# Optimization experiments

Hardware: AMD Instinct MI355X
Metric: run time of the kernel (lower is better)

Reference implementation:

```python
import jax, jax.numpy as jnp
import numpy as np

D = 64       # d_model (channel)
NHEAD = 8    # heads in nn.MultiheadAttention
PROTO = 16   # proto_size == num_queries
EPS = 1e-5


def _haar_filters():
    L = np.array([1.0, 1.0], np.float32) / np.float32(np.sqrt(2.0))
    H = np.array([-1.0, 1.0], np.float32) / np.float32(np.sqrt(2.0))
    # WavePool: LL, LH, HL, HH Haar filters (2x2, stride 2, depthwise)
    return [jnp.asarray(np.outer(a, b)) for (a, b) in ((L, L), (L, H), (H, L), (H, H))]


def _dw(x, k2d, stride):
    # depthwise conv with the SAME 2D filter per channel; x: [B,C,H,W]
    C = x.shape[1]
    k = jnp.tile(k2d[None, None], (C, 1, 1, 1)).astype(x.dtype)
    return jax.lax.conv_general_dilated(x, k, (stride, stride), 'VALID',
        dimension_numbers=('NCHW', 'OIHW', 'NCHW'), feature_group_count=C)


def _ln(x, g, b):
    m = jnp.mean(x, -1, keepdims=True)
    v = jnp.var(x, -1, keepdims=True)
    return (x - m) * jax.lax.rsqrt(v + EPS) * g + b


def _bn(x, g, b, m, v):
    # eval-mode BatchNorm2d, x: [B,C,H,W]
    sh = (1, -1, 1, 1)
    return (x - m.reshape(sh)) * jax.lax.rsqrt(v.reshape(sh) + EPS) * g.reshape(sh) + b.reshape(sh)


def _mscw(x, lw1, lb1, lw2, lb2, gw1, gb1, gw2, gb2):
    pool = jnp.mean(x, axis=1, keepdims=True)            # [B,1,C]
    loc = jax.nn.relu(x @ lw1.T + lb1) @ lw2.T + lb2
    glo = jax.nn.relu(pool @ gw1.T + gb1) @ gw2.T + gb2
    return jax.nn.sigmoid(loc + glo)


def _mha(q, k, v, w_in, b_in, w_out, b_out):
    # standard nn.MultiheadAttention (batch_first), q:[B,Nq,D], k/v:[B,Nk,D]
    B, Nq, d = q.shape
    dk = d // NHEAD
    qp = q @ w_in[:d].T + b_in[:d]
    kp = k @ w_in[d:2 * d].T + b_in[d:2 * d]
    vp = v @ w_in[2 * d:].T + b_in[2 * d:]
    split = lambda t: t.reshape(t.shape[0], t.shape[1], NHEAD, dk).transpose(0, 2, 1, 3)
    qh, kh, vh = split(qp), split(kp), split(vp)
    scores = jnp.einsum('bhqd,bhkd->bhqk', qh, kh) * (1.0 / np.sqrt(dk))
    attn = jax.nn.softmax(scores, axis=-1)
    o = jnp.einsum('bhqk,bhkd->bhqd', attn, vh).transpose(0, 2, 1, 3).reshape(B, Nq, d)
    return o @ w_out.T + b_out


def reference(tgt, memory, pos, query_pos,
              w_in, b_in, w_out, b_out,
              ln1_g, ln1_b, ln2_g, ln2_b,
              m1_lw1, m1_lb1, m1_lw2, m1_lb2, m1_gw1, m1_gb1, m1_gw2, m1_gb2,
              m2_lw1, m2_lb1, m2_lw2, m2_lb2, m2_gw1, m2_gb1, m2_gw2, m2_gb2,
              dw_w, bn1_g, bn1_b, bn1_m, bn1_v, pw_w, bn2_g, bn2_b, bn2_m, bn2_v,
              mheads_w):
    # CrossAttentionLayer.forward_post -> custom MultiheadAttention.forward
    query = (tgt + query_pos).transpose(1, 0, 2)   # [B,Nq,C]
    key = (memory + pos).transpose(1, 0, 2)        # [B,N1,C]
    value = memory.transpose(1, 0, 2)
    B, N1, C = value.shape
    hw = int(np.sqrt(N1))
    feat = key.transpose(0, 2, 1).reshape(B, C, hw, hw)
    fLL, fLH, fHL, fHH = _haar_filters()
    LL = _dw(feat, fLL, 2)
    LH = _dw(feat, fLH, 2)
    HL = _dw(feat, fHL, 2)
    HH = _dw(feat, fHH, 2)
    high = (HL + LH + HH).reshape(B, C, -1).transpose(0, 2, 1)  # [B,N1/4,C]
    low = LL.reshape(B, C, -1).transpose(0, 2, 1)
    wei = _mscw(high + low, m1_lw1, m1_lb1, m1_lw2, m1_lb2, m1_gw1, m1_gb1, m1_gw2, m1_gb2)
    fre = wei * high + low
    x1 = _mha(query, fre, fre, w_in, b_in, w_out, b_out)
    x1 = _ln(x1 + query, ln1_g, ln1_b)
    # DSConv3x3: depthwise 3x3 + BN + ReLU, then 1x1 + BN + ReLU
    y = jax.lax.conv_general_dilated(feat, dw_w, (1, 1), ((1, 1), (1, 1)),
        dimension_numbers=('NCHW', 'OIHW', 'NCHW'), feature_group_count=C)
    y = jax.nn.relu(_bn(y, bn1_g, bn1_b, bn1_m, bn1_v))
    y = jax.lax.conv_general_dilated(y, pw_w, (1, 1), 'VALID',
        dimension_numbers=('NCHW', 'OIHW', 'NCHW'))
    y = jax.nn.relu(_bn(y, bn2_g, bn2_b, bn2_m, bn2_v))
    featf = y.reshape(B, C, -1).transpose(0, 2, 1)          # [B,N1,C]
    mw = jax.nn.softmax(featf @ mheads_w.T, axis=1)          # softmax over tokens, [B,N1,P]
    protos = jnp.einsum('bnp,bnc->bpc', mw, key)             # [B,P,C]
    attn2 = _mscw(protos + query, m2_lw1, m2_lb1, m2_lw2, m2_lb2, m2_gw1, m2_gb1, m2_gw2, m2_gb2)
    x2 = _ln(query * attn2 + query, ln2_g, ln2_b)
    return (x1 + x2).transpose(1, 0, 2)                      # [Nq,B,C]


def setup_inputs() -> dict:
    key = jax.random.key(0)
    ks = iter(jax.random.split(key, 40))
    B, HW, NQ = 8, 128, PROTO
    N1 = HW * HW
    wn = lambda *s: jax.random.normal(next(ks), s, jnp.float32) * 0.05
    inp = {
        'tgt': jax.random.normal(next(ks), (NQ, B, D), jnp.float32),
        'memory': jax.random.normal(next(ks), (N1, B, D), jnp.float32),
        'pos': jax.random.normal(next(ks), (N1, B, D), jnp.float32),
        'query_pos': jax.random.normal(next(ks), (NQ, B, D), jnp.float32),
        'w_in': wn(3 * D, D), 'b_in': jnp.zeros((3 * D,), jnp.float32),
        'w_out': wn(D, D), 'b_out': jnp.zeros((D,), jnp.float32),
        'ln1_g': jnp.ones((D,), jnp.float32), 'ln1_b': jnp.zeros((D,), jnp.float32),
        'ln2_g': jnp.ones((D,), jnp.float32), 'ln2_b': jnp.zeros((D,), jnp.float32),
        'dw_w': wn(D, 1, 3, 3),
        'bn1_g': jnp.ones((D,), jnp.float32), 'bn1_b': jnp.zeros((D,), jnp.float32),
        'bn1_m': jnp.zeros((D,), jnp.float32), 'bn1_v': jnp.ones((D,), jnp.float32),
        'pw_w': wn(D, D, 1, 1),
        'bn2_g': jnp.ones((D,), jnp.float32), 'bn2_b': jnp.zeros((D,), jnp.float32),
        'bn2_m': jnp.zeros((D,), jnp.float32), 'bn2_v': jnp.ones((D,), jnp.float32),
        'mheads_w': wn(PROTO, D),
    }
    for pfx in ('m1', 'm2'):
        for br in ('l', 'g'):
            inp[f'{pfx}_{br}w1'] = wn(D, D)
            inp[f'{pfx}_{br}b1'] = jnp.zeros((D,), jnp.float32)
            inp[f'{pfx}_{br}w2'] = wn(D, D)
            inp[f'{pfx}_{br}b2'] = jnp.zeros((D,), jnp.float32)
    return inp
```

## Files before the change

### kernel.cpp

```cpp
#include <hip/hip_runtime.h>
#include <math.h>

#define N1 16384
#define N2 4096

#define OFF_KEY   0L
#define OFF_KPH   4194304L
#define OFF_VPH   5242880L
#define OFF_WB    6291456L
#define OFF_CST   6302208L
#define OFF_POOL  6331648L
#define OFF_PROT  6332160L
#define OFF_ZZ    6340352L
#define OFF_QP    6340480L
#define OFF_QB    6348672L
#define OFF_PART  6356864L

typedef __attribute__((ext_vector_type(8))) short bf16x8;
typedef __attribute__((ext_vector_type(4))) float floatx4;

#define MFMA16(a, b, c) __builtin_amdgcn_mfma_f32_16x16x32_bf16(a, b, c, 0, 0, 0)

__device__ __forceinline__ unsigned short f2bf(float f) {
    union { float f; unsigned u; } v; v.f = f;
    unsigned r = v.u + 0x7fffu + ((v.u >> 16) & 1u);
    return (unsigned short)(r >> 16);
}
__device__ __forceinline__ float bf2f(unsigned short s) {
    union { unsigned u; float f; } v; v.u = ((unsigned)s) << 16;
    return v.f;
}
__device__ __forceinline__ float sigmoidf_(float x) { return 1.f / (1.f + __expf(-x)); }
__device__ __forceinline__ bf16x8 ldg8b(const unsigned short* p) { return *(const bf16x8*)p; }
__device__ __forceinline__ void unpack8(uint4 v, float* f) {
    f[0] = bf2f((unsigned short)(v.x & 0xffff)); f[1] = bf2f((unsigned short)(v.x >> 16));
    f[2] = bf2f((unsigned short)(v.y & 0xffff)); f[3] = bf2f((unsigned short)(v.y >> 16));
    f[4] = bf2f((unsigned short)(v.z & 0xffff)); f[5] = bf2f((unsigned short)(v.z >> 16));
    f[6] = bf2f((unsigned short)(v.w & 0xffff)); f[7] = bf2f((unsigned short)(v.w >> 16));
}

__global__ __launch_bounds__(256) void k_stage1(
        const float* __restrict__ mem, const float* __restrict__ pos,
        const float* __restrict__ m1lw1, const float* __restrict__ m1lw2,
        const float* __restrict__ w_in, const float* __restrict__ pw,
        const float* __restrict__ mh, const float* __restrict__ dw_w,
        const float* __restrict__ bn1_g, const float* __restrict__ bn1_b,
        const float* __restrict__ bn1_m, const float* __restrict__ bn1_v,
        const float* __restrict__ bn2_g, const float* __restrict__ bn2_b,
        const float* __restrict__ bn2_m, const float* __restrict__ bn2_v,
        const float* __restrict__ m1gw1, const float* __restrict__ m1gw2,
        const float* __restrict__ m2gw1, const float* __restrict__ m2gw2,
        const float* __restrict__ m2lw1, const float* __restrict__ m2lw2,
        const float* __restrict__ w_out,
        const float* __restrict__ tgt, const float* __restrict__ qpos,
        const float* __restrict__ b_in,
        unsigned short* __restrict__ key, float* __restrict__ pool1raw,
        unsigned short* __restrict__ wb, float* __restrict__ cst,
        float* __restrict__ qp, float* __restrict__ queryb) {
    int tid = threadIdx.x;
    if (blockIdx.x < 4096) {
        __shared__ float sh[16][64];
        int b = blockIdx.x >> 9;
        int n_base = (blockIdx.x & 511) * 32;
        int c8 = tid & 7, local_n = tid >> 3;
        int n = n_base + local_n;
        long s4 = ((long)n * 8 + b) * 16 + c8 * 2;
        float4 m0 = ((const float4*)mem)[s4], m1 = ((const float4*)mem)[s4 + 1];
        float4 p0 = ((const float4*)pos)[s4], p1 = ((const float4*)pos)[s4 + 1];
        float f[8];
        f[0] = m0.x + p0.x; f[1] = m0.y + p0.y; f[2] = m0.z + p0.z; f[3] = m0.w + p0.w;
        f[4] = m1.x + p1.x; f[5] = m1.y + p1.y; f[6] = m1.z + p1.z; f[7] = m1.w + p1.w;
        uint4 o;
        o.x = (unsigned)f2bf(f[0]) | ((unsigned)f2bf(f[1]) << 16);
        o.y = (unsigned)f2bf(f[2]) | ((unsigned)f2bf(f[3]) << 16);
        o.z = (unsigned)f2bf(f[4]) | ((unsigned)f2bf(f[5]) << 16);
        o.w = (unsigned)f2bf(f[6]) | ((unsigned)f2bf(f[7]) << 16);
        ((uint4*)key)[(long)(b * 16384 + n) * 8 + c8] = o;
        int parity = (n_base >> 7) & 1;
        if (parity) {
            if (local_n & 1) {
                #pragma unroll
                for (int j = 0; j < 8; j++) sh[local_n >> 1][c8 * 8 + j] = f[j];
            }
            __syncthreads();
            if (tid < 64) {
                float s = 0.f;
                #pragma unroll
                for (int k = 0; k < 16; k++) s += sh[k][tid];
                atomicAdd(pool1raw + b * 64 + tid, s);
            }
        }
        return;
    }
    int blk = blockIdx.x - 4096;
    if (blk < 84) {
        int i = blk * 256 + tid;
        float v;
        if (i < 4096) v = m1lw1[i];
        else if (i < 8192) v = m1lw2[i - 4096];
        else if (i < 16384) v = w_in[4096 + (i - 8192)];
        else if (i < 20480) v = pw[i - 16384];
        else v = mh[i - 20480];
        wb[i] = f2bf(v);
    } else if (blk < 199) {
        int j = (blk - 84) * 256 + tid;
        float v;
        if (j < 576) {
            int k = j >> 6, c = j & 63;
            float s1 = bn1_g[c] * rsqrtf(bn1_v[c] + 1e-5f);
            v = dw_w[c * 9 + k] * s1;
        } else if (j < 640) {
            int c = j - 576;
            float s1 = bn1_g[c] * rsqrtf(bn1_v[c] + 1e-5f);
            v = bn1_b[c] - bn1_m[c] * s1;
        } else if (j < 704) {
            int c = j - 640;
            v = bn2_g[c] * rsqrtf(bn2_v[c] + 1e-5f);
        } else if (j < 768) {
            int c = j - 704;
            float s2 = bn2_g[c] * rsqrtf(bn2_v[c] + 1e-5f);
            v = bn2_b[c] - bn2_m[c] * s2;
        } else {
            int jj = j - 768;
            int m = jj >> 12, idx = jj & 4095;
            int sidx = (idx & 63) * 64 + (idx >> 6);
            const float* src;
            switch (m) {
                case 0: src = m1gw1; break;
                case 1: src = m1gw2; break;
                case 2: src = m2gw1; break;
                case 3: src = m2gw2; break;
                case 4: src = m2lw1; break;
                case 5: src = m2lw2; break;
                default: src = w_out; break;
            }
            v = src[sidx];
        }
        cst[j] = v;
    } else {
        __shared__ float qv[4][64];
        int g = tid >> 6, lane = tid & 63;
        int u = (blk - 199) * 4 + g;
        int b = u >> 4, q = u & 15;
        long src = ((long)q * 8 + b) * 64 + lane;
        float v = tgt[src] + qpos[src];
        qv[g][lane] = v;
        queryb[(b * 16 + q) * 64 + lane] = v;
        __syncthreads();
        float acc = b_in[lane];
        for (int cc = 0; cc < 64; cc++) acc += qv[g][cc] * w_in[lane * 64 + cc];
        qp[(b * 16 + q) * 64 + lane] = acc;
    }
}

__global__ __launch_bounds__(512) void k_stage2(
        const unsigned short* __restrict__ keyb,
        const float* __restrict__ pool1raw,
        const float* __restrict__ lb1, const float* __restrict__ lb2,
        const float* __restrict__ gb1, const float* __restrict__ gb2,
        const float* __restrict__ b_in,
        const unsigned short* __restrict__ wb,
        const float* __restrict__ cst,
        unsigned short* __restrict__ kph, unsigned short* __restrict__ vph,
        float* __restrict__ protos, float* __restrict__ Z) {
    __shared__ __align__(16) char smem[63488];
    int tid = threadIdx.x;
    int w = tid >> 6, l = tid & 63;
    if (blockIdx.x < 512) {
        short* stage = (short*)smem;
        short* hbuf  = (short*)(smem + 36864);
        short* wbuf  = (short*)(smem + 46080);
        float* parr  = (float*)(smem + 55296);
        float* gtmp  = parr + 64;
        float* gbuf  = parr + 128;
        int b = blockIdx.x >> 6, tile = blockIdx.x & 63;
        int pairw = w >> 1, ch2 = w & 1;
        int m0 = pairw * 16, trow = l & 15, oct = l >> 4;
        const float* gw1T = cst + 768;
        const float* gw2T = cst + 4864;
        if (tid < 64) parr[tid] = pool1raw[b * 64 + tid] * (2.0f / 4096.0f);
        const unsigned short* src = keyb + ((long)b * 16384 + tile * 256) * 64;
        #pragma unroll
        for (int k = 0; k < 4; k++) {
            int u = k * 512 + tid;
            int p = u >> 3, o = u & 7;
            uint4 v = *(const uint4*)(src + (long)u * 8);
            *(uint4*)(stage + p * 72 + o * 8) = v;
        }
        __syncthreads();
        if (tid < 64) {
            float a = gb1[tid];
            for (int cc = 0; cc < 64; cc++) a += parr[cc] * gw1T[cc * 64 + tid];
            gtmp[tid] = fmaxf(a, 0.f);
        }
        int j = m0 + trow;
        float x[16], S[16];
        bf16x8 ax[2];
        #pragma unroll
        for (int half = 0; half < 2; half++) {
            int o = oct + half * 4;
            uint4 fa4 = *(const uint4*)(stage + (2 * j) * 72 + o * 8);
            uint4 fb4 = *(const uint4*)(stage + (2 * j + 1) * 72 + o * 8);
            uint4 fc4 = *(const uint4*)(stage + (128 + 2 * j) * 72 + o * 8);
            uint4 fd4 = *(const uint4*)(stage + (129 + 2 * j) * 72 + o * 8);
            float A[8], B[8], C[8], D[8];
            unpack8(fa4, A); unpack8(fb4, B); unpack8(fc4, C); unpack8(fd4, D);
            #pragma unroll
            for (int jj = 0; jj < 8; jj++) {
                float xd = 2.f * D[jj];
                x[half * 8 + jj] = xd;
                S[half * 8 + jj] = 0.5f * (A[jj] + B[jj] + C[jj] + D[jj]);
                ax[half][jj] = (short)f2bf(xd);
            }
        }
        const unsigned short* w1b = wb;
        const unsigned short* w2b = wb + 4096;
        const unsigned short* wkb = wb + 8192;
        const unsigned short* wvb = wb + 12288;
        #pragma unroll
        for (int t4i = 0; t4i < 2; t4i++) {
            int n = (ch2 * 2 + t4i) * 16 + trow;
            float bias = lb1[n];
            floatx4 acc = {bias, bias, bias, bias};
            acc = MFMA16(ax[0], ldg8b(w1b + n * 64 + oct * 8), acc);
            acc = MFMA16(ax[1], ldg8b(w1b + n * 64 + 32 + oct * 8), acc);
            #pragma unroll
            for (int r = 0; r < 4; r++)
                hbuf[(m0 + oct * 4 + r) * 72 + n] = (short)f2bf(fmaxf(acc[r], 0.f));
        }
        __syncthreads();
        if (tid < 64) {
            float g = gb2[tid];
            for (int hh = 0; hh < 64; hh++) g += gtmp[hh] * gw2T[hh * 64 + tid];
            gbuf[tid] = g;
        }
        __syncthreads();
        {
            bf16x8 ah0 = *(const bf16x8*)(hbuf + (m0 + trow) * 72 + oct * 8);
            bf16x8 ah1 = *(const bf16x8*)(hbuf + (m0 + trow) * 72 + 32 + oct * 8);
            #pragma unroll
            for (int t4i = 0; t4i < 2; t4i++) {
                int n = (ch2 * 2 + t4i) * 16 + trow;
                float bias = lb2[n];
                floatx4 acc = {bias, bias, bias, bias};
                acc = MFMA16(ah0, ldg8b(w2b + n * 64 + oct * 8), acc);
                acc = MFMA16(ah1, ldg8b(w2b + n * 64 + 32 + oct * 8), acc);
                float g = gbuf[n];
                #pragma unroll
                for (int r = 0; r < 4; r++)
                    wbuf[(m0 + oct * 4 + r) * 72 + n] = (short)f2bf(sigmoidf_(acc[r] + g));
            }
        }
        __syncthreads();
        bf16x8 af0, af1;
        {
            bf16x8 w0 = *(const bf16x8*)(wbuf + (m0 + trow) * 72 + oct * 8);
            bf16x8 w1v = *(const bf16x8*)(wbuf + (m0 + trow) * 72 + 32 + oct * 8);
            #pragma unroll
            for (int jj = 0; jj < 8; jj++) {
                float we0 = bf2f((unsigned short)w0[jj]);
                float we1 = bf2f((unsigned short)w1v[jj]);
                af0[jj] = (short)f2bf(we0 * x[jj] + (1.f - we0) * S[jj]);
                af1[jj] = (short)f2bf(we1 * x[8 + jj] + (1.f - we1) * S[8 + jj]);
            }
        }
        __syncthreads();
        short* kbuf = hbuf; short* vbuf = wbuf;
        #pragma unroll
        for (int t4i = 0; t4i < 2; t4i++) {
            int ko = (ch2 * 2 + t4i) * 16 + trow;
            float bk = b_in[64 + ko], bv = b_in[128 + ko];
            floatx4 ak = {bk, bk, bk, bk};
            floatx4 av = {bv, bv, bv, bv};
            ak = MFMA16(af0, ldg8b(wkb + ko * 64 + oct * 8), ak);
            ak = MFMA16(af1, ldg8b(wkb + ko * 64 + 32 + oct * 8), ak);
            av = MFMA16(af0, ldg8b(wvb + ko * 64 + oct * 8), av);
            av = MFMA16(af1, ldg8b(wvb + ko * 64 + 32 + oct * 8), av);
            #pragma unroll
            for (int r = 0; r < 4; r++) {
                int row = m0 + oct * 4 + r;
                kbuf[row * 72 + ko] = (short)f2bf(ak[r]);
                vbuf[row * 72 + ko] = (short)f2bf(av[r]);
            }
        }
        __syncthreads();
        {
            int h = tid >> 6, tok = tid & 63;
            uint4 kk = *(const uint4*)(kbuf + tok * 72 + h * 8);
            uint4 vv = *(const uint4*)(vbuf + tok * 72 + h * 8);
            long du = (long)(b * 8 + h) * 4096 + tile * 64 + tok;
            ((uint4*)kph)[du] = kk;
            ((uint4*)vph)[du] = vv;
        }
        return;
    }
    {
        short* stage = (short*)smem;
        short* pbuf  = (short*)(smem + 55296);
        float* cbuf  = (float*)(smem + 55296 + 4352);
        float* zred  = (float*)(smem + 55296 + 4352 + 3072);
        int blk = blockIdx.x - 512;
        int b = blk >> 7, h = blk & 127;
        int p0 = w * 16, pr = l & 15, oct = l >> 4;
        for (int k = tid; k < 768; k += 512) cbuf[k] = cst[k];
        const unsigned short* kb = keyb + (long)b * 1048576;
        #pragma unroll
        for (int r = 0; r < 3; r++) {
            int row = h - 1 + r;
            if ((unsigned)row < 128u) {
                const unsigned short* src = kb + (long)row * 8192;
                #pragma unroll
                for (int k = 0; k < 2; k++) {
                    int u = k * 512 + tid;
                    int p = u >> 3, o = u & 7;
                    uint4 v = *(const uint4*)(src + (long)u * 8);
                    *(uint4*)(stage + (r * 128 + p) * 72 + o * 8) = v;
                }
            } else {
                uint4 zz = {0u, 0u, 0u, 0u};
                #pragma unroll
                for (int k = 0; k < 2; k++) {
                    int u = k * 512 + tid;
                    int p = u >> 3, o = u & 7;
                    *(uint4*)(stage + (r * 128 + p) * 72 + o * 8) = zz;
                }
            }
        }
        __syncthreads();
        float accf[2][8];
        #pragma unroll
        for (int half = 0; half < 2; half++)
            #pragma unroll
            for (int jj = 0; jj < 8; jj++) accf[half][jj] = 0.f;
        #pragma unroll
        for (int r = 0; r < 3; r++) {
            #pragma unroll
            for (int kk = 0; kk < 3; kk++) {
                int col = p0 + pr - 1 + kk;
                if ((unsigned)col < 128u) {
                    #pragma unroll
                    for (int half = 0; half < 2; half++) {
                        int o = oct + half * 4;
                        uint4 d4 = *(const uint4*)(stage + (r * 128 + col) * 72 + o * 8);
                        float f[8]; unpack8(d4, f);
                        float4 wa = *(const float4*)(cbuf + (r * 3 + kk) * 64 + o * 8);
                        float4 wc = *(const float4*)(cbuf + (r * 3 + kk) * 64 + o * 8 + 4);
                        accf[half][0] += f[0] * wa.x; accf[half][1] += f[1] * wa.y;
                        accf[half][2] += f[2] * wa.z; accf[half][3] += f[3] * wa.w;
                        accf[half][4] += f[4] * wc.x; accf[half][5] += f[5] * wc.y;
                        accf[half][6] += f[6] * wc.z; accf[half][7] += f[7] * wc.w;
                    }
                }
            }
        }
        bf16x8 af[2];
        #pragma unroll
        for (int half = 0; half < 2; half++) {
            int o = oct + half * 4;
            float4 oa = *(const float4*)(cbuf + 576 + o * 8);
            float4 ob = *(const float4*)(cbuf + 576 + o * 8 + 4);
            af[half][0] = (short)f2bf(fmaxf(accf[half][0] + oa.x, 0.f));
            af[half][1] = (short)f2bf(fmaxf(accf[half][1] + oa.y, 0.f));
            af[half][2] = (short)f2bf(fmaxf(accf[half][2] + oa.z, 0.f));
            af[half][3] = (short)f2bf(fmaxf(accf[half][3] + oa.w, 0.f));
            af[half][4] = (short)f2bf(fmaxf(accf[half][4] + ob.x, 0.f));
            af[half][5] = (short)f2bf(fmaxf(accf[half][5] + ob.y, 0.f));
            af[half][6] = (short)f2bf(fmaxf(accf[half][6] + ob.z, 0.f));
            af[half][7] = (short)f2bf(fmaxf(accf[half][7] + ob.w, 0.f));
        }
        __syncthreads();
        short* y2buf = stage;
        short* KT = stage + 18432;
        {
            const unsigned short* pwb = wb + 16384;
            #pragma unroll
            for (int t4 = 0; t4 < 4; t4++) {
                int n = t4 * 16 + pr;
                floatx4 acc = {0.f, 0.f, 0.f, 0.f};
                acc = MFMA16(af[0], ldg8b(pwb + n * 64 + oct * 8), acc);
                acc = MFMA16(af[1], ldg8b(pwb + n * 64 + 32 + oct * 8), acc);
                float s2 = cbuf[640 + n], o2 = cbuf[704 + n];
                #pragma unroll
                for (int r = 0; r < 4; r++)
                    y2buf[(p0 + oct * 4 + r) * 72 + n] = (short)f2bf(fmaxf(acc[r] * s2 + o2, 0.f));
            }
            #pragma unroll
            for (int k = 0; k < 2; k++) {
                int u = k * 512 + tid;
                int n = u >> 3, o = u & 7;
                uint4 v = *(const uint4*)(stage + (128 + n) * 72 + o * 8);
                int nx = n ^ (o << 3);
                KT[(o * 8 + 0) * 136 + nx] = (short)(v.x & 0xffff);
                KT[(o * 8 + 1) * 136 + nx] = (short)(v.x >> 16);
                KT[(o * 8 + 2) * 136 + nx] = (short)(v.y & 0xffff);
                KT[(o * 8 + 3) * 136 + nx] = (short)(v.y >> 16);
                KT[(o * 8 + 4) * 136 + nx] = (short)(v.z & 0xffff);
                KT[(o * 8 + 5) * 136 + nx] = (short)(v.z >> 16);
                KT[(o * 8 + 6) * 136 + nx] = (short)(v.w & 0xffff);
                KT[(o * 8 + 7) * 136 + nx] = (short)(v.w >> 16);
            }
        }
        __syncthreads();
        {
            const unsigned short* mhb = wb + 20480;
            bf16x8 a0 = *(const bf16x8*)(y2buf + (p0 + pr) * 72 + oct * 8);
            bf16x8 a1 = *(const bf16x8*)(y2buf + (p0 + pr) * 72 + 32 + oct * 8);
            floatx4 lg = {0.f, 0.f, 0.f, 0.f};
            lg = MFMA16(a0, ldg8b(mhb + pr * 64 + oct * 8), lg);
            lg = MFMA16(a1, ldg8b(mhb + pr * 64 + 32 + oct * 8), lg);
            float zs = 0.f;
            #pragma unroll
            for (int r = 0; r < 4; r++) {
                float e = __expf(lg[r]);
                zs += e;
                pbuf[pr * 136 + p0 + oct * 4 + r] = (short)f2bf(e);
            }
            zs += __shfl_xor(zs, 16);
            zs += __shfl_xor(zs, 32);
            if (l < 16) zred[w * 16 + l] = zs;
        }
        __syncthreads();
        if (w < 4) {
            int c = w * 16 + pr;
            int xrc = ((c >> 3) & 7) << 3;
            floatx4 acc = {0.f, 0.f, 0.f, 0.f};
            #pragma unroll
            for (int s = 0; s < 4; s++) {
                bf16x8 A = *(const bf16x8*)(pbuf + pr * 136 + s * 32 + oct * 8);
                bf16x8 B = *(const bf16x8*)(KT + c * 136 + ((s * 32 + oct * 8) ^ xrc));
                acc = MFMA16(A, B, acc);
            }
            #pragma unroll
            for (int r = 0; r < 4; r++)
                atomicAdd(protos + (b * 16 + oct * 4 + r) * 64 + c, acc[r]);
        }
        if (tid < 16) {
            float zt = 0.f;
            #pragma unroll
            for (int ww = 0; ww < 8; ww++) zt += zred[ww * 16 + tid];
            atomicAdd(Z + b * 16 + tid, zt);
        }
    }
}

__global__ __launch_bounds__(256) void k_mha(const float* __restrict__ qp,
                                             const unsigned short* __restrict__ kph,
                                             const unsigned short* __restrict__ vph,
                                             float* __restrict__ part) {
    int bh = blockIdx.x >> 3, seg = blockIdx.x & 7;
    int b = bh >> 3, hh = bh & 7;
    int tid = threadIdx.x;
    int q = tid >> 4, sub = tid & 15;
    const float* qv = qp + (long)(b * 16 + q) * 64 + hh * 8;
    float4 q0 = ((const float4*)qv)[0];
    float4 q1 = ((const float4*)qv)[1];
    const uint4* K4 = (const uint4*)kph + (long)bh * 4096;
    const uint4* V4 = (const uint4*)vph + (long)bh * 4096;
    const float scale = 0.35355339059327373f;
    float m = -1e30f, lsum = 0.f;
    float acc[8];
    #pragma unroll
    for (int d = 0; d < 8; d++) acc[d] = 0.f;
    for (int i = 0; i < 32; i++) {
        int n = seg * 512 + i * 16 + sub;
        float k8[8]; unpack8(K4[n], k8);
        float s = q0.x * k8[0] + q0.y * k8[1] + q0.z * k8[2] + q0.w * k8[3]
                + q1.x * k8[4] + q1.y * k8[5] + q1.z * k8[6] + q1.w * k8[7];
        s *= scale;
        float nm = fmaxf(m, s);
        float corr = __expf(m - nm);
        float wgt = __expf(s - nm);
        lsum = lsum * corr + wgt;
        float v8[8]; unpack8(V4[n], v8);
        #pragma unroll
        for (int d = 0; d < 8; d++) acc[d] = acc[d] * corr + wgt * v8[d];
        m = nm;
    }
    #pragma unroll
    for (int off = 1; off < 16; off <<= 1) {
        float om = __shfl_xor(m, off);
        float ol = __shfl_xor(lsum, off);
        float oa[8];
        #pragma unroll
        for (int d = 0; d < 8; d++) oa[d] = __shfl_xor(acc[d], off);
        float nm = fmaxf(m, om);
        float c1 = __expf(m - nm), c2 = __expf(om - nm);
        lsum = lsum * c1 + ol * c2;
        #pragma unroll
        for (int d = 0; d < 8; d++) acc[d] = acc[d] * c1 + oa[d] * c2;
        m = nm;
    }
    if (sub == 0) {
        float* P = part + ((long)(bh * 16 + q) * 8 + seg) * 12;
        P[0] = m; P[1] = lsum;
        #pragma unroll
        for (int d = 0; d < 8; d++) P[2 + d] = acc[d];
    }
}

__global__ __launch_bounds__(1024) void k_final(
        const float* __restrict__ queryb, const float* __restrict__ protos,
        const float* __restrict__ Z, const float* __restrict__ part,
        const float* __restrict__ cst,
        const float* __restrict__ b_out,
        const float* __restrict__ ln1_g, const float* __restrict__ ln1_b,
        const float* __restrict__ ln2_g, const float* __restrict__ ln2_b,
        const float* __restrict__ lb1, const float* __restrict__ lb2,
        const float* __restrict__ gb1, const float* __restrict__ gb2,
        float* __restrict__ out) {
    const float* gw1T = cst + 8960;
    const float* gw2T = cst + 13056;
    const float* lw1T = cst + 17152;
    const float* lw2T = cst + 21248;
    const float* woT  = cst + 25344;
    int b = blockIdx.x;
    int t = threadIdx.x >> 6;
    int c = threadIdx.x & 63;
    __shared__ float xs[16][64], hid[16][64], os[16][64];
    __shared__ float pool[64], hidg[64], glo[64];
    float q = queryb[(long)(b * 16 + t) * 64 + c];
    float rz = 1.f / Z[b * 16 + t];
    float xin = protos[(long)(b * 16 + t) * 64 + c] * rz + q;
    xs[t][c] = xin;
    {
        int hh = c >> 3, d = c & 7;
        const float* P = part + ((long)((b * 8 + hh) * 16 + t) * 8) * 12;
        float mm = -1e30f, ll = 0.f, aa = 0.f;
        #pragma unroll
        for (int s = 0; s < 8; s++) {
            float pm = P[s * 12], pl2 = P[s * 12 + 1], pa = P[s * 12 + 2 + d];
            float nm = fmaxf(mm, pm);
            float c1 = __expf(mm - nm), c2 = __expf(pm - nm);
            aa = aa * c1 + pa * c2;
            ll = ll * c1 + pl2 * c2;
            mm = nm;
        }
        os[t][c] = aa / ll;
    }
    __syncthreads();
    if (threadIdx.x < 64) {
        float s = 0.f;
        for (int tt = 0; tt < 16; tt++) s += xs[tt][threadIdx.x];
        pool[threadIdx.x] = s * (1.f / 16.f);
    }
    __syncthreads();
    if (threadIdx.x < 64) {
        int hh = threadIdx.x;
        float a = gb1[hh];
        for (int cc = 0; cc < 64; cc++) a += pool[cc] * gw1T[cc * 64 + hh];
        hidg[hh] = fmaxf(a, 0.f);
    }
    __syncthreads();
    if (threadIdx.x < 64) {
        int ccc = threadIdx.x;
        float a = gb2[ccc];
        for (int hh = 0; hh < 64; hh++) a += hidg[hh] * gw2T[hh * 64 + ccc];
        glo[ccc] = a;
    }
    float a = lb1[c];
    for (int cc = 0; cc < 64; cc++) a += xs[t][cc] * lw1T[cc * 64 + c];
    hid[t][c] = fmaxf(a, 0.f);
    __syncthreads();
    float loc = lb2[c];
    for (int hh = 0; hh < 64; hh++) loc += hid[t][hh] * lw2T[hh * 64 + c];
    float attn2 = sigmoidf_(loc + glo[c]);
    float x2p = q * attn2 + q;
    float mu = x2p;
    for (int off = 32; off; off >>= 1) mu += __shfl_down(mu, off);
    mu = __shfl(mu, 0) * (1.f / 64.f);
    float d0 = x2p - mu;
    float vv = d0 * d0;
    for (int off = 32; off; off >>= 1) vv += __shfl_down(vv, off);
    vv = __shfl(vv, 0) * (1.f / 64.f);
    float x2 = d0 * rsqrtf(vv + 1e-5f) * ln2_g[c] + ln2_b[c];
    float x1p = b_out[c];
    for (int k = 0; k < 64; k++) x1p += os[t][k] * woT[k * 64 + c];
    x1p += q;
    float mu1 = x1p;
    for (int off = 32; off; off >>= 1) mu1 += __shfl_down(mu1, off);
    mu1 = __shfl(mu1, 0) * (1.f / 64.f);
    float d1 = x1p - mu1;
    float v1 = d1 * d1;
    for (int off = 32; off; off >>= 1) v1 += __shfl_down(v1, off);
    v1 = __shfl(v1, 0) * (1.f / 64.f);
    float x1 = d1 * rsqrtf(v1 + 1e-5f) * ln1_g[c] + ln1_b[c];
    out[((long)t * 8 + b) * 64 + c] = x1 + x2;
}

extern "C" void kernel_launch(void* const* d_in, const int* in_sizes, int n_in,
                              void* d_out, int out_size, void* d_ws, size_t ws_size,
                              hipStream_t stream) {
    const float* tgt       = (const float*)d_in[0];
    const float* memory    = (const float*)d_in[1];
    const float* pos       = (const float*)d_in[2];
    const float* query_pos = (const float*)d_in[3];
    const float* w_in      = (const float*)d_in[4];
    const float* b_in      = (const float*)d_in[5];
    const float* w_out     = (const float*)d_in[6];
    const float* b_out     = (const float*)d_in[7];
    const float* ln1_g     = (const float*)d_in[8];
    const float* ln1_b     = (const float*)d_in[9];
    const float* ln2_g     = (const float*)d_in[10];
    const float* ln2_b     = (const float*)d_in[11];
    const float* dw_w      = (const float*)d_in[12];
    const float* bn1_g     = (const float*)d_in[13];
    const float* bn1_b     = (const float*)d_in[14];
    const float* bn1_m     = (const float*)d_in[15];
    const float* bn1_v     = (const float*)d_in[16];
    const float* pw_w      = (const float*)d_in[17];
    const float* bn2_g     = (const float*)d_in[18];
    const float* bn2_b     = (const float*)d_in[19];
    const float* bn2_m     = (const float*)d_in[20];
    const float* bn2_v     = (const float*)d_in[21];
    const float* mheads    = (const float*)d_in[22];
    const float* m1_lw1 = (const float*)d_in[23];
    const float* m1_lb1 = (const float*)d_in[24];
    const float* m1_lw2 = (const float*)d_in[25];
    const float* m1_lb2 = (const float*)d_in[26];
    const float* m1_gw1 = (const float*)d_in[27];
    const float* m1_gb1 = (const float*)d_in[28];
    const float* m1_gw2 = (const float*)d_in[29];
    const float* m1_gb2 = (const float*)d_in[30];
    const float* m2_lw1 = (const float*)d_in[31];
    const float* m2_lb1 = (const float*)d_in[32];
    const float* m2_lw2 = (const float*)d_in[33];
    const float* m2_lb2 = (const float*)d_in[34];
    const float* m2_gw1 = (const float*)d_in[35];
    const float* m2_gb1 = (const float*)d_in[36];
    const float* m2_gw2 = (const float*)d_in[37];
    const float* m2_gb2 = (const float*)d_in[38];

    float* ws = (float*)d_ws;
    float* out = (float*)d_out;
    unsigned short* keyb = (unsigned short*)(ws + OFF_KEY);
    unsigned short* kph  = (unsigned short*)(ws + OFF_KPH);
    unsigned short* vph  = (unsigned short*)(ws + OFF_VPH);
    unsigned short* wb   = (unsigned short*)(ws + OFF_WB);

    hipMemsetAsync(ws + OFF_POOL, 0, 8832 * sizeof(float), stream);

    k_stage1<<<4327, 256, 0, stream>>>(memory, pos,
                                       m1_lw1, m1_lw2, w_in, pw_w, mheads, dw_w,
                                       bn1_g, bn1_b, bn1_m, bn1_v,
                                       bn2_g, bn2_b, bn2_m, bn2_v,
                                       m1_gw1, m1_gw2, m2_gw1, m2_gw2,
                                       m2_lw1, m2_lw2, w_out,
                                       tgt, query_pos, b_in,
                                       keyb, ws + OFF_POOL, wb, ws + OFF_CST,
                                       ws + OFF_QP, ws + OFF_QB);
    k_stage2<<<1536, 512, 0, stream>>>(keyb, ws + OFF_POOL,
                                       m1_lb1, m1_lb2, m1_gb1, m1_gb2, b_in,
                                       wb, ws + OFF_CST,
                                       kph, vph, ws + OFF_PROT, ws + OFF_ZZ);
    k_mha<<<512, 256, 0, stream>>>(ws + OFF_QP, kph, vph, ws + OFF_PART);
    k_final<<<8, 1024, 0, stream>>>(ws + OFF_QB, ws + OFF_PROT, ws + OFF_ZZ, ws + OFF_PART,
                                    ws + OFF_CST, b_out,
                                    ln1_g, ln1_b, ln2_g, ln2_b,
                                    m2_lb1, m2_lb2, m2_gb1, m2_gb2,
                                    out);
}
```

Before: 243.4 us.

## Fuse cross-attention into stage2 via atomic softmax partial sums; drop k_mha

The K/V projection tiles produced in k_stage2 are no longer written to global memory. Attention over each 64-token tile is computed in the same block, and unnormalized exp-sums and weighted values are accumulated into a small global buffer with atomicAdd. This removes the k_mha launch and the K/V round trip through global memory. k_final is regridded to 128 blocks of 64 threads. The trade-off is that the running-max subtraction is dropped, so exp may overflow for large scores, and results depend on atomic ordering.

```diff
diff --git a/kernel.cpp b/kernel.cpp
--- a/kernel.cpp
+++ b/kernel.cpp
@@ -2,19 +2,16 @@
 #include <math.h>
 
 #define N1 16384
-#define N2 4096
 
 #define OFF_KEY   0L
-#define OFF_KPH   4194304L
-#define OFF_VPH   5242880L
-#define OFF_WB    6291456L
-#define OFF_CST   6302208L
-#define OFF_POOL  6331648L
-#define OFF_PROT  6332160L
-#define OFF_ZZ    6340352L
-#define OFF_QP    6340480L
-#define OFF_QB    6348672L
-#define OFF_PART  6356864L
+#define OFF_WB    4194304L
+#define OFF_CST   4205056L
+#define OFF_POOL  4234496L
+#define OFF_PROT  4235008L
+#define OFF_ZZ    4243200L
+#define OFF_OSUM  4243328L
+#define OFF_QP    4255616L
+#define OFF_QB    4263808L
 
 typedef __attribute__((ext_vector_type(8))) short bf16x8;
 typedef __attribute__((ext_vector_type(4))) float floatx4;
@@ -161,7 +158,8 @@
         const float* __restrict__ b_in,
         const unsigned short* __restrict__ wb,
         const float* __restrict__ cst,
-        unsigned short* __restrict__ kph, unsigned short* __restrict__ vph,
+        const float* __restrict__ qp,
+        float* __restrict__ osum,
         float* __restrict__ protos, float* __restrict__ Z) {
     __shared__ __align__(16) char smem[63488];
     int tid = threadIdx.x;
@@ -173,12 +171,19 @@
         float* parr  = (float*)(smem + 55296);
         float* gtmp  = parr + 64;
         float* gbuf  = parr + 128;
+        float* qs    = (float*)(smem + 56064);
         int b = blockIdx.x >> 6, tile = blockIdx.x & 63;
         int pairw = w >> 1, ch2 = w & 1;
         int m0 = pairw * 16, trow = l & 15, oct = l >> 4;
         const float* gw1T = cst + 768;
         const float* gw2T = cst + 4864;
         if (tid < 64) parr[tid] = pool1raw[b * 64 + tid] * (2.0f / 4096.0f);
+        {
+            int i0 = tid;
+            qs[(i0 >> 6) * 68 + (i0 & 63)] = qp[(b * 16 + (i0 >> 6)) * 64 + (i0 & 63)];
+            int i1 = tid + 512;
+            qs[(i1 >> 6) * 68 + (i1 & 63)] = qp[(b * 16 + (i1 >> 6)) * 64 + (i1 & 63)];
+        }
         const unsigned short* src = keyb + ((long)b * 16384 + tile * 256) * 64;
         #pragma unroll
         for (int k = 0; k < 4; k++) {
@@ -285,12 +290,42 @@
         }
         __syncthreads();
         {
-            int h = tid >> 6, tok = tid & 63;
-            uint4 kk = *(const uint4*)(kbuf + tok * 72 + h * 8);
-            uint4 vv = *(const uint4*)(vbuf + tok * 72 + h * 8);
-            long du = (long)(b * 8 + h) * 4096 + tile * 64 + tok;
-            ((uint4*)kph)[du] = kk;
-            ((uint4*)vph)[du] = vv;
+            int h = w;
+            int q = l & 15, grp = l >> 4;
+            float qf[8];
+            #pragma unroll
+            for (int d = 0; d < 8; d++) qf[d] = qs[q * 68 + h * 8 + d];
+            const float scale = 0.35355339059327373f;
+            float lsum = 0.f, acc[8];
+            #pragma unroll
+            for (int d = 0; d < 8; d++) acc[d] = 0.f;
+            #pragma unroll
+            for (int ti = 0; ti < 16; ti++) {
+                int tok = grp * 16 + ti;
+                uint4 k4 = *(const uint4*)(kbuf + tok * 72 + h * 8);
+                uint4 v4 = *(const uint4*)(vbuf + tok * 72 + h * 8);
+                float kf[8], vf[8];
+                unpack8(k4, kf); unpack8(v4, vf);
+                float s = qf[0] * kf[0] + qf[1] * kf[1] + qf[2] * kf[2] + qf[3] * kf[3]
+                        + qf[4] * kf[4] + qf[5] * kf[5] + qf[6] * kf[6] + qf[7] * kf[7];
+                float e = __expf(s * scale);
+                lsum += e;
+                #pragma unroll
+                for (int d = 0; d < 8; d++) acc[d] += e * vf[d];
+            }
+            lsum += __shfl_xor(lsum, 16);
+            lsum += __shfl_xor(lsum, 32);
+            #pragma unroll
+            for (int d = 0; d < 8; d++) {
+                acc[d] += __shfl_xor(acc[d], 16);
+                acc[d] += __shfl_xor(acc[d], 32);
+            }
+            if (grp == 0) {
+                float* P = osum + ((long)((b * 8 + h) * 16 + q)) * 12;
+                atomicAdd(P, lsum);
+                #pragma unroll
+                for (int d = 0; d < 8; d++) atomicAdd(P + 1 + d, acc[d]);
+            }
         }
         return;
     }
@@ -385,8 +420,8 @@
                     y2buf[(p0 + oct * 4 + r) * 72 + n] = (short)f2bf(fmaxf(acc[r] * s2 + o2, 0.f));
             }
             #pragma unroll
-            for (int k = 0; k < 2; k++) {
-                int u = k * 512 + tid;
+            for (int k2 = 0; k2 < 2; k2++) {
+                int u = k2 * 512 + tid;
                 int n = u >> 3, o = u & 7;
                 uint4 v = *(const uint4*)(stage + (128 + n) * 72 + o * 8);
                 int nx = n ^ (o << 3);
@@ -443,64 +478,9 @@
     }
 }
 
-__global__ __launch_bounds__(256) void k_mha(const float* __restrict__ qp,
-                                             const unsigned short* __restrict__ kph,
-                                             const unsigned short* __restrict__ vph,
-                                             float* __restrict__ part) {
-    int bh = blockIdx.x >> 3, seg = blockIdx.x & 7;
-    int b = bh >> 3, hh = bh & 7;
-    int tid = threadIdx.x;
-    int q = tid >> 4, sub = tid & 15;
-    const float* qv = qp + (long)(b * 16 + q) * 64 + hh * 8;
-    float4 q0 = ((const float4*)qv)[0];
-    float4 q1 = ((const float4*)qv)[1];
-    const uint4* K4 = (const uint4*)kph + (long)bh * 4096;
-    const uint4* V4 = (const uint4*)vph + (long)bh * 4096;
-    const float scale = 0.35355339059327373f;
-    float m = -1e30f, lsum = 0.f;
-    float acc[8];
-    #pragma unroll
-    for (int d = 0; d < 8; d++) acc[d] = 0.f;
-    for (int i = 0; i < 32; i++) {
-        int n = seg * 512 + i * 16 + sub;
-        float k8[8]; unpack8(K4[n], k8);
-        float s = q0.x * k8[0] + q0.y * k8[1] + q0.z * k8[2] + q0.w * k8[3]
-                + q1.x * k8[4] + q1.y * k8[5] + q1.z * k8[6] + q1.w * k8[7];
-        s *= scale;
-        float nm = fmaxf(m, s);
-        float corr = __expf(m - nm);
-        float wgt = __expf(s - nm);
-        lsum = lsum * corr + wgt;
-        float v8[8]; unpack8(V4[n], v8);
-        #pragma unroll
-        for (int d = 0; d < 8; d++) acc[d] = acc[d] * corr + wgt * v8[d];
-        m = nm;
-    }
-    #pragma unroll
-    for (int off = 1; off < 16; off <<= 1) {
-        float om = __shfl_xor(m, off);
-        float ol = __shfl_xor(lsum, off);
-        float oa[8];
-        #pragma unroll
-        for (int d = 0; d < 8; d++) oa[d] = __shfl_xor(acc[d], off);
-        float nm = fmaxf(m, om);
-        float c1 = __expf(m - nm), c2 = __expf(om - nm);
-        lsum = lsum * c1 + ol * c2;
-        #pragma unroll
-        for (int d = 0; d < 8; d++) acc[d] = acc[d] * c1 + oa[d] * c2;
-        m = nm;
-    }
-    if (sub == 0) {
-        float* P = part + ((long)(bh * 16 + q) * 8 + seg) * 12;
-        P[0] = m; P[1] = lsum;
-        #pragma unroll
-        for (int d = 0; d < 8; d++) P[2 + d] = acc[d];
-    }
-}
-
-__global__ __launch_bounds__(1024) void k_final(
+__global__ __launch_bounds__(64) void k_final(
         const float* __restrict__ queryb, const float* __restrict__ protos,
-        const float* __restrict__ Z, const float* __restrict__ part,
+        const float* __restrict__ Z, const float* __restrict__ osum,
         const float* __restrict__ cst,
         const float* __restrict__ b_out,
         const float* __restrict__ ln1_g, const float* __restrict__ ln1_b,
@@ -513,58 +493,44 @@
     const float* lw1T = cst + 17152;
     const float* lw2T = cst + 21248;
     const float* woT  = cst + 25344;
-    int b = blockIdx.x;
-    int t = threadIdx.x >> 6;
-    int c = threadIdx.x & 63;
-    __shared__ float xs[16][64], hid[16][64], os[16][64];
-    __shared__ float pool[64], hidg[64], glo[64];
-    float q = queryb[(long)(b * 16 + t) * 64 + c];
-    float rz = 1.f / Z[b * 16 + t];
-    float xin = protos[(long)(b * 16 + t) * 64 + c] * rz + q;
-    xs[t][c] = xin;
+    int b = blockIdx.x >> 4, t = blockIdx.x & 15;
+    int c = threadIdx.x;
+    __shared__ float pool[64], xsrow[64], hid[64], hidg[64], osv[64];
+    float q_own = queryb[(long)(b * 16 + t) * 64 + c];
+    float poolacc = 0.f, xin_own = 0.f;
+    #pragma unroll
+    for (int tt = 0; tt < 16; tt++) {
+        float rz = 1.f / Z[b * 16 + tt];
+        float xv = protos[(long)(b * 16 + tt) * 64 + c] * rz
+                 + queryb[(long)(b * 16 + tt) * 64 + c];
+        poolacc += xv;
+        if (tt == t) xin_own = xv;
+    }
+    pool[c] = poolacc * (1.f / 16.f);
+    xsrow[c] = xin_own;
     {
         int hh = c >> 3, d = c & 7;
-        const float* P = part + ((long)((b * 8 + hh) * 16 + t) * 8) * 12;
-        float mm = -1e30f, ll = 0.f, aa = 0.f;
-        #pragma unroll
-        for (int s = 0; s < 8; s++) {
-            float pm = P[s * 12], pl2 = P[s * 12 + 1], pa = P[s * 12 + 2 + d];
-            float nm = fmaxf(mm, pm);
-            float c1 = __expf(mm - nm), c2 = __expf(pm - nm);
-            aa = aa * c1 + pa * c2;
-            ll = ll * c1 + pl2 * c2;
-            mm = nm;
-        }
-        os[t][c] = aa / ll;
+        const float* P = osum + ((long)((b * 8 + hh) * 16 + t)) * 12;
+        osv[c] = P[1 + d] / P[0];
     }
     __syncthreads();
-    if (threadIdx.x < 64) {
-        float s = 0.f;
-        for (int tt = 0; tt < 16; tt++) s += xs[tt][threadIdx.x];
-        pool[threadIdx.x] = s * (1.f / 16.f);
+    {
+        float a = gb1[c], a2 = lb1[c];
+        for (int cc = 0; cc < 64; cc++) {
+            a  += pool[cc]  * gw1T[cc * 64 + c];
+            a2 += xsrow[cc] * lw1T[cc * 64 + c];
+        }
+        hidg[c] = fmaxf(a, 0.f);
+        hid[c]  = fmaxf(a2, 0.f);
     }
     __syncthreads();
-    if (threadIdx.x < 64) {
-        int hh = threadIdx.x;
-        float a = gb1[hh];
-        for (int cc = 0; cc < 64; cc++) a += pool[cc] * gw1T[cc * 64 + hh];
-        hidg[hh] = fmaxf(a, 0.f);
-    }
-    __syncthreads();
-    if (threadIdx.x < 64) {
-        int ccc = threadIdx.x;
-        float a = gb2[ccc];
-        for (int hh = 0; hh < 64; hh++) a += hidg[hh] * gw2T[hh * 64 + ccc];
-        glo[ccc] = a;
-    }
-    float a = lb1[c];
-    for (int cc = 0; cc < 64; cc++) a += xs[t][cc] * lw1T[cc * 64 + c];
-    hid[t][c] = fmaxf(a, 0.f);
-    __syncthreads();
-    float loc = lb2[c];
-    for (int hh = 0; hh < 64; hh++) loc += hid[t][hh] * lw2T[hh * 64 + c];
-    float attn2 = sigmoidf_(loc + glo[c]);
-    float x2p = q * attn2 + q;
+    float glo = gb2[c], loc = lb2[c];
+    for (int hh = 0; hh < 64; hh++) {
+        glo += hidg[hh] * gw2T[hh * 64 + c];
+        loc += hid[hh]  * lw2T[hh * 64 + c];
+    }
+    float attn2 = sigmoidf_(loc + glo);
+    float x2p = q_own * attn2 + q_own;
     float mu = x2p;
     for (int off = 32; off; off >>= 1) mu += __shfl_down(mu, off);
     mu = __shfl(mu, 0) * (1.f / 64.f);
@@ -574,8 +540,8 @@
     vv = __shfl(vv, 0) * (1.f / 64.f);
     float x2 = d0 * rsqrtf(vv + 1e-5f) * ln2_g[c] + ln2_b[c];
     float x1p = b_out[c];
-    for (int k = 0; k < 64; k++) x1p += os[t][k] * woT[k * 64 + c];
-    x1p += q;
+    for (int k = 0; k < 64; k++) x1p += osv[k] * woT[k * 64 + c];
+    x1p += q_own;
     float mu1 = x1p;
     for (int off = 32; off; off >>= 1) mu1 += __shfl_down(mu1, off);
     mu1 = __shfl(mu1, 0) * (1.f / 64.f);
@@ -633,11 +599,9 @@
     float* ws = (float*)d_ws;
     float* out = (float*)d_out;
     unsigned short* keyb = (unsigned short*)(ws + OFF_KEY);
-    unsigned short* kph  = (unsigned short*)(ws + OFF_KPH);
-    unsigned short* vph  = (unsigned short*)(ws + OFF_VPH);
     unsigned short* wb   = (unsigned short*)(ws + OFF_WB);
 
-    hipMemsetAsync(ws + OFF_POOL, 0, 8832 * sizeof(float), stream);
+    hipMemsetAsync(ws + OFF_POOL, 0, 21120 * sizeof(float), stream);
 
     k_stage1<<<4327, 256, 0, stream>>>(memory, pos,
                                        m1_lw1, m1_lw2, w_in, pw_w, mheads, dw_w,
@@ -650,10 +614,9 @@
                                        ws + OFF_QP, ws + OFF_QB);
     k_stage2<<<1536, 512, 0, stream>>>(keyb, ws + OFF_POOL,
                                        m1_lb1, m1_lb2, m1_gb1, m1_gb2, b_in,
-                                       wb, ws + OFF_CST,
-                                       kph, vph, ws + OFF_PROT, ws + OFF_ZZ);
-    k_mha<<<512, 256, 0, stream>>>(ws + OFF_QP, kph, vph, ws + OFF_PART);
-    k_final<<<8, 1024, 0, stream>>>(ws + OFF_QB, ws + OFF_PROT, ws + OFF_ZZ, ws + OFF_PART,
+                                       wb, ws + OFF_CST, ws + OFF_QP,
+                                       ws + OFF_OSUM, ws + OFF_PROT, ws + OFF_ZZ);
+    k_final<<<128, 64, 0, stream>>>(ws + OFF_QB, ws + OFF_PROT, ws + OFF_ZZ, ws + OFF_OSUM,
                                     ws + OFF_CST, b_out,
                                     ln1_g, ln1_b, ln2_g, ln2_b,
                                     m2_lb1, m2_lb2, m2_gb1, m2_gb2,
```

After: 261.6 us. 1.07x slower.
